# Kernel tuning notes

Hardware: AMD Instinct MI355X
Metric: run time of the kernel (lower is better)

The kernel has to match this reference:

```python
import jax, jax.numpy as jnp
import numpy as np

R_ITER = 3
EPS = 1e-7  # keras.backend.epsilon()


def squash(v, axis=-1):
    s2 = jnp.sum(jnp.square(v), axis=axis, keepdims=True)
    scale = s2 / (1.0 + s2) / jnp.sqrt(s2 + EPS)
    return scale * v


def setup_inputs() -> dict:
    key = jax.random.key(0)
    kx, kw = jax.random.split(key)
    B, N_IN, D_IN = 64, 2048, 8
    N_OUT, D_OUT = 32, 16
    x = jax.random.normal(kx, (B, N_IN, D_IN), dtype=jnp.float32)
    # W matches keras weight (1, N_IN//shared, N_OUT, D_OUT, D_IN) with shared=1,
    # stored here without the leading broadcast dim. RandomNormal(stddev=0.1).
    W = 0.1 * jax.random.normal(kw, (N_IN, N_OUT, D_OUT, D_IN), dtype=jnp.float32)
    return {"x": x, "W": W}


def reference(x, W):
    # predictions u_hat[b, i, j, :] = W[i, j] @ x[b, i]  -> [B, N_in, N_out, D_out]
    preds = jnp.einsum('nodi,bni->bnod', W, x)
    N_in, N_out = preds.shape[1], preds.shape[2]
    # raw routing logits start at zeros with broadcast batch dim (as in TF code)
    raw = jnp.zeros((1, N_in, N_out), dtype=x.dtype)
    for i in range(R_ITER):
        rw = jax.nn.softmax(raw, axis=2)                      # softmax over output caps
        s = jnp.sum(rw[..., None] * preds, axis=1)            # [B, N_out, D_out]
        v = squash(s, axis=-1)                                # squash over capsule dim
        if i < R_ITER - 1:
            # agreement: <u_hat_ij, v_j>
            raw = raw + jnp.einsum('bnod,bod->bno', preds, v)
    return v, rw
```

## Files before the change

kernel.cpp:

```cpp
#include <hip/hip_runtime.h>

static constexpr int B_    = 64;
static constexpr int N_    = 2048;
static constexpr int DI_   = 8;
static constexpr int O_    = 32;
static constexpr int P_    = 16;
static constexpr int OP_   = O_ * P_;
static constexpr int M_    = OP_ * B_;
static constexpr int CHUNK_ = 8;
static constexpr int NBLK_  = N_ / CHUNK_;
static constexpr int WSLICE_ = O_ * P_ * DI_;

template <int CTRL>
__device__ __forceinline__ float dpp_add(float v) {
  int t = __builtin_amdgcn_update_dpp(0, __float_as_int(v), CTRL, 0xf, 0xf, false);
  return v + __int_as_float(t);
}

__device__ __forceinline__ float rfl(float v) {
  return __int_as_float(__builtin_amdgcn_readfirstlane(__float_as_int(v)));
}

template <int MODE, bool ATOMIC>
__global__ __launch_bounds__(512, 2)
void fused_pass(const float* __restrict__ x, const float* __restrict__ W,
                const float* __restrict__ v_in, float* __restrict__ s_out,
                float* __restrict__ rw_out) {
  __shared__ __align__(16) float w_lds[WSLICE_];
  const int tid  = threadIdx.x;
  const int lane = tid & 63;
  const int wu   = __builtin_amdgcn_readfirstlane(tid >> 6);
  const int o    = lane >> 1;
  const int ph   = lane & 1;
  const int cn   = blockIdx.x >> 1;
  const int bh   = blockIdx.x & 1;
  const int n0   = cn * CHUNK_;
  const int b0   = bh * 32 + wu * 4;

  const int t2  = tid + 512;
  const int sw0 = (tid ^ ((tid >> 4) & 7)) * 4;
  const int sw1 = (t2  ^ ((t2  >> 4) & 7)) * 4;
  const int wbase = lane * 64 + (lane & 7) * 4;

  float s_r[4][8];
  #pragma unroll
  for (int bb = 0; bb < 4; ++bb)
    #pragma unroll
    for (int pp = 0; pp < 8; ++pp) s_r[bb][pp] = 0.0f;

  {
    const float4 a = *(const float4*)(W + (size_t)n0 * WSLICE_ + tid * 4);
    const float4 b = *(const float4*)(W + (size_t)n0 * WSLICE_ + t2 * 4);
    *(float4*)&w_lds[sw0] = a;
    *(float4*)&w_lds[sw1] = b;
  }
  __syncthreads();

  #pragma unroll 1
  for (int nn = 0; nn < CHUNK_; ++nn) {
    const int n = n0 + nn;

    float4 wrA, wrB;
    if (nn + 1 < CHUNK_) {
      wrA = *(const float4*)(W + (size_t)(n + 1) * WSLICE_ + tid * 4);
      wrB = *(const float4*)(W + (size_t)(n + 1) * WSLICE_ + t2 * 4);
    }

    float xs[4][8];
    #pragma unroll
    for (int bb = 0; bb < 4; ++bb) {
      const float* xp = x + (size_t)(b0 + bb) * (N_ * DI_) + (size_t)n * DI_;
      const float4 xa = *(const float4*)xp;
      const float4 xc = *(const float4*)(xp + 4);
      xs[bb][0] = rfl(xa.x); xs[bb][1] = rfl(xa.y);
      xs[bb][2] = rfl(xa.z); xs[bb][3] = rfl(xa.w);
      xs[bb][4] = rfl(xc.x); xs[bb][5] = rfl(xc.y);
      xs[bb][6] = rfl(xc.z); xs[bb][7] = rfl(xc.w);
    }

    float pr[4][8];
    #pragma unroll
    for (int pp = 0; pp < 8; ++pp) {
      const float4 w0 = *(const float4*)&w_lds[wbase ^ (8 * pp)];
      const float4 w1 = *(const float4*)&w_lds[wbase ^ (8 * pp + 4)];
      #pragma unroll
      for (int bb = 0; bb < 4; ++bb) {
        float pv = w0.x * xs[bb][0];
        pv = __builtin_fmaf(w0.y, xs[bb][1], pv);
        pv = __builtin_fmaf(w0.z, xs[bb][2], pv);
        pv = __builtin_fmaf(w0.w, xs[bb][3], pv);
        pv = __builtin_fmaf(w1.x, xs[bb][4], pv);
        pv = __builtin_fmaf(w1.y, xs[bb][5], pv);
        pv = __builtin_fmaf(w1.z, xs[bb][6], pv);
        pv = __builtin_fmaf(w1.w, xs[bb][7], pv);
        if (MODE == 0) s_r[bb][pp] += pv;
        else           pr[bb][pp] = pv;
      }
    }

    if (MODE != 0) {
      #pragma unroll
      for (int bb = 0; bb < 4; ++bb) {
        const float4* vp = (const float4*)(v_in + (size_t)(b0 + bb) * OP_ +
                                           o * P_ + ph * 8);
        const float4 va = vp[0];
        const float4 vc = vp[1];
        float acc = pr[bb][0] * va.x;
        acc = __builtin_fmaf(pr[bb][1], va.y, acc);
        acc = __builtin_fmaf(pr[bb][2], va.z, acc);
        acc = __builtin_fmaf(pr[bb][3], va.w, acc);
        acc = __builtin_fmaf(pr[bb][4], vc.x, acc);
        acc = __builtin_fmaf(pr[bb][5], vc.y, acc);
        acc = __builtin_fmaf(pr[bb][6], vc.z, acc);
        acc = __builtin_fmaf(pr[bb][7], vc.w, acc);
        const float full = dpp_add<0xB1>(acc);
        const float e = __expf(full);
        float srow = e;
        srow = dpp_add<0x121>(srow);
        srow = dpp_add<0x122>(srow);
        srow = dpp_add<0x124>(srow);
        srow = dpp_add<0x128>(srow);
        float t16 = srow + __shfl_xor(srow, 16);
        const float S = t16 + __shfl_xor(t16, 32);
        const float rw = (2.0f * e) / S;
        #pragma unroll
        for (int pp = 0; pp < 8; ++pp)
          s_r[bb][pp] = __builtin_fmaf(rw, pr[bb][pp], s_r[bb][pp]);
        if (MODE == 2) {
          if (ph == 0)
            rw_out[((size_t)(b0 + bb) * N_ + n) * O_ + o] = rw;
        }
      }
    }

    if (nn + 1 < CHUNK_) {
      __syncthreads();
      *(float4*)&w_lds[sw0] = wrA;
      *(float4*)&w_lds[sw1] = wrB;
      __syncthreads();
    }
  }

  if (ATOMIC) {
    #pragma unroll
    for (int bb = 0; bb < 4; ++bb) {
      #pragma unroll
      for (int h = 0; h < 2; ++h)
        #pragma unroll
        for (int j = 0; j < 4; ++j)
          atomicAdd(&s_out[(size_t)(b0 + bb) * 512 + h * 256 + lane * 4 + j],
                    s_r[bb][h * 4 + j]);
    }
  } else {
    #pragma unroll
    for (int bb = 0; bb < 4; ++bb) {
      float* sp = s_out + (size_t)cn * M_ + (size_t)(b0 + bb) * 512 + lane * 4;
      float4 st0, st1;
      st0.x = s_r[bb][0]; st0.y = s_r[bb][1]; st0.z = s_r[bb][2]; st0.w = s_r[bb][3];
      st1.x = s_r[bb][4]; st1.y = s_r[bb][5]; st1.z = s_r[bb][6]; st1.w = s_r[bb][7];
      *(float4*)sp = st0;
      *(float4*)(sp + 256) = st1;
    }
  }
}

__global__ __launch_bounds__(1024)
void reduce1(const float* __restrict__ spart, float* __restrict__ p2, int K) {
  const int g  = blockIdx.x >> 4;
  const int mc = blockIdx.x & 15;
  const int kpg = K >> 4;
  const int m0 = mc * 2048 + threadIdx.x;
  float a0 = 0.0f, a1 = 0.0f;
  const float* p = spart + (size_t)(g * kpg) * M_;
  for (int k = 0; k < kpg; ++k) {
    a0 += p[(size_t)k * M_ + m0];
    a1 += p[(size_t)k * M_ + m0 + 1024];
  }
  p2[(size_t)g * M_ + m0]        = a0;
  p2[(size_t)g * M_ + m0 + 1024] = a1;
}

__global__ __launch_bounds__(1024)
void v_kernel(const float* __restrict__ src, int ngroups, float scale,
              const float* __restrict__ v_add, float* __restrict__ v_out,
              float* __restrict__ zero_buf) {
  __shared__ float sq[P_ * 65];
  const int t = threadIdx.x;
  const int p = t & 15;
  const int b = t >> 4;
  const int o = blockIdx.x;
  const int q = o * P_ + p;
  const int idx_src = b * 512 + ((p >> 2) & 1) * 256 + (2 * o + (p >> 3)) * 4 +
                      (p & 3);
  float acc = 0.0f;
  for (int g = 0; g < ngroups; ++g)
    acc += src[(size_t)g * M_ + idx_src];
  acc *= scale;
  sq[p * 65 + b] = acc * acc;
  if (zero_buf) zero_buf[blockIdx.x * 1024 + t] = 0.0f;
  __syncthreads();
  float s2 = 0.0f;
  #pragma unroll
  for (int pp = 0; pp < P_; ++pp) s2 += sq[pp * 65 + b];
  float sc = (s2 / (1.0f + s2)) / sqrtf(s2 + 1e-7f);
  float v = acc * sc;
  const int idx = b * OP_ + q;
  v_out[idx] = v + (v_add ? v_add[idx] : 0.0f);
}

extern "C" void kernel_launch(void* const* d_in, const int* in_sizes, int n_in,
                              void* d_out, int out_size, void* d_ws, size_t ws_size,
                              hipStream_t stream) {
  (void)in_sizes; (void)n_in; (void)out_size;
  const float* x = (const float*)d_in[0];
  const float* W = (const float*)d_in[1];
  float* out_v  = (float*)d_out;
  float* out_rw = out_v + (size_t)B_ * O_ * P_;
  float* vws   = (float*)d_ws;
  float* vsum  = vws + M_;
  float* p2    = vsum + M_;
  float* spart = p2 + 16 * M_;

  const size_t need = (size_t)(2 * M_ + 16 * M_ + (size_t)NBLK_ * M_) * 4;

  dim3 gF(2 * NBLK_), bF(512), gV(O_), bV(1024), gR(256), bR(1024);
  if (ws_size >= need) {
    fused_pass<0, false><<<gF, bF, 0, stream>>>(x, W, nullptr, spart, nullptr);
    reduce1<<<gR, bR, 0, stream>>>(spart, p2, NBLK_);
    v_kernel<<<gV, bV, 0, stream>>>(p2, 16, 1.0f / 32.0f, nullptr, vws, nullptr);
    fused_pass<1, false><<<gF, bF, 0, stream>>>(x, W, vws, spart, nullptr);
    reduce1<<<gR, bR, 0, stream>>>(spart, p2, NBLK_);
    v_kernel<<<gV, bV, 0, stream>>>(p2, 16, 1.0f, vws, vsum, nullptr);
    fused_pass<2, false><<<gF, bF, 0, stream>>>(x, W, vsum, spart, out_rw);
    reduce1<<<gR, bR, 0, stream>>>(spart, p2, NBLK_);
    v_kernel<<<gV, bV, 0, stream>>>(p2, 16, 1.0f, nullptr, out_v, nullptr);
  } else {
    float* sAb = p2;
    float* sBb = sAb + M_;
    hipMemsetAsync(sAb, 0, (size_t)M_ * sizeof(float), stream);
    fused_pass<0, true><<<gF, bF, 0, stream>>>(x, W, nullptr, sAb, nullptr);
    v_kernel<<<gV, bV, 0, stream>>>(sAb, 1, 1.0f / 32.0f, nullptr, vws, sBb);
    fused_pass<1, true><<<gF, bF, 0, stream>>>(x, W, vws, sBb, nullptr);
    v_kernel<<<gV, bV, 0, stream>>>(sBb, 1, 1.0f, vws, vsum, sAb);
    fused_pass<2, true><<<gF, bF, 0, stream>>>(x, W, vsum, sAb, out_rw);
    v_kernel<<<gV, bV, 0, stream>>>(sAb, 1, 1.0f, nullptr, out_v, nullptr);
  }
}
```

Measured before the change: 224.6 us.

## Double-buffer W in LDS, stage x in LDS, split batch into quarters

Each block now has 256 threads and covers a quarter of the batch, so the grid has four times as many blocks. The W slice is double-buffered in LDS, which drops one of the two barriers per iteration. Each block's x tile is loaded into LDS once up front instead of being read from global memory every iteration, and the v_in loads are hoisted ahead of the dot products. In exchange, each W slice is fetched by four blocks instead of two, and LDS use per block roughly doubles, which could limit occupancy.

```diff
diff --git a/kernel.cpp b/kernel.cpp
--- a/kernel.cpp
+++ b/kernel.cpp
@@ -22,24 +22,24 @@
 }
 
 template <int MODE, bool ATOMIC>
-__global__ __launch_bounds__(512, 2)
+__global__ __launch_bounds__(256, 4)
 void fused_pass(const float* __restrict__ x, const float* __restrict__ W,
                 const float* __restrict__ v_in, float* __restrict__ s_out,
                 float* __restrict__ rw_out) {
-  __shared__ __align__(16) float w_lds[WSLICE_];
+  __shared__ __align__(16) float w_lds[2][WSLICE_];
+  __shared__ __align__(16) float x_lds[16 * 64];
   const int tid  = threadIdx.x;
   const int lane = tid & 63;
   const int wu   = __builtin_amdgcn_readfirstlane(tid >> 6);
   const int o    = lane >> 1;
   const int ph   = lane & 1;
-  const int cn   = blockIdx.x >> 1;
-  const int bh   = blockIdx.x & 1;
+  const int cn   = blockIdx.x >> 2;
+  const int bq   = blockIdx.x & 3;
   const int n0   = cn * CHUNK_;
-  const int b0   = bh * 32 + wu * 4;
-
-  const int t2  = tid + 512;
-  const int sw0 = (tid ^ ((tid >> 4) & 7)) * 4;
-  const int sw1 = (t2  ^ ((t2  >> 4) & 7)) * 4;
+  const int b0_blk = bq * 16;
+  const int b0w  = b0_blk + wu * 4;
+
+  const int swk = (tid ^ ((tid >> 4) & 7)) * 4;
   const int wbase = lane * 64 + (lane & 7) * 4;
 
   float s_r[4][8];
@@ -49,29 +49,41 @@
     for (int pp = 0; pp < 8; ++pp) s_r[bb][pp] = 0.0f;
 
   {
-    const float4 a = *(const float4*)(W + (size_t)n0 * WSLICE_ + tid * 4);
-    const float4 b = *(const float4*)(W + (size_t)n0 * WSLICE_ + t2 * 4);
-    *(float4*)&w_lds[sw0] = a;
-    *(float4*)&w_lds[sw1] = b;
+    const int bl = tid >> 4;
+    const int ch = tid & 15;
+    const float4 xv = *(const float4*)(
+        x + (size_t)(b0_blk + bl) * (N_ * DI_) + n0 * DI_ + ch * 4);
+    *(float4*)&x_lds[bl * 64 + ch * 4] = xv;
+    #pragma unroll
+    for (int k = 0; k < 4; ++k) {
+      const float4 wv =
+          *(const float4*)(W + (size_t)n0 * WSLICE_ + (tid + k * 256) * 4);
+      *(float4*)&w_lds[0][swk + k * 1024] = wv;
+    }
   }
   __syncthreads();
 
   #pragma unroll 1
   for (int nn = 0; nn < CHUNK_; ++nn) {
     const int n = n0 + nn;
-
-    float4 wrA, wrB;
+    const float* wbuf = w_lds[nn & 1];
+    float* wnxt = w_lds[(nn + 1) & 1];
+
+    float4 wr0, wr1, wr2, wr3;
     if (nn + 1 < CHUNK_) {
-      wrA = *(const float4*)(W + (size_t)(n + 1) * WSLICE_ + tid * 4);
-      wrB = *(const float4*)(W + (size_t)(n + 1) * WSLICE_ + t2 * 4);
+      const float* wp = W + (size_t)(n + 1) * WSLICE_ + tid * 4;
+      wr0 = *(const float4*)(wp);
+      wr1 = *(const float4*)(wp + 1024);
+      wr2 = *(const float4*)(wp + 2048);
+      wr3 = *(const float4*)(wp + 3072);
     }
 
     float xs[4][8];
     #pragma unroll
     for (int bb = 0; bb < 4; ++bb) {
-      const float* xp = x + (size_t)(b0 + bb) * (N_ * DI_) + (size_t)n * DI_;
-      const float4 xa = *(const float4*)xp;
-      const float4 xc = *(const float4*)(xp + 4);
+      const int xb = (wu * 4 + bb) * 64 + nn * 8;
+      const float4 xa = *(const float4*)&x_lds[xb];
+      const float4 xc = *(const float4*)&x_lds[xb + 4];
       xs[bb][0] = rfl(xa.x); xs[bb][1] = rfl(xa.y);
       xs[bb][2] = rfl(xa.z); xs[bb][3] = rfl(xa.w);
       xs[bb][4] = rfl(xc.x); xs[bb][5] = rfl(xc.y);
@@ -81,8 +93,8 @@
     float pr[4][8];
     #pragma unroll
     for (int pp = 0; pp < 8; ++pp) {
-      const float4 w0 = *(const float4*)&w_lds[wbase ^ (8 * pp)];
-      const float4 w1 = *(const float4*)&w_lds[wbase ^ (8 * pp + 4)];
+      const float4 w0 = *(const float4*)&wbuf[wbase ^ (8 * pp)];
+      const float4 w1 = *(const float4*)&wbuf[wbase ^ (8 * pp + 4)];
       #pragma unroll
       for (int bb = 0; bb < 4; ++bb) {
         float pv = w0.x * xs[bb][0];
@@ -99,20 +111,24 @@
     }
 
     if (MODE != 0) {
+      float4 va[4], vc[4];
       #pragma unroll
       for (int bb = 0; bb < 4; ++bb) {
-        const float4* vp = (const float4*)(v_in + (size_t)(b0 + bb) * OP_ +
-                                           o * P_ + ph * 8);
-        const float4 va = vp[0];
-        const float4 vc = vp[1];
-        float acc = pr[bb][0] * va.x;
-        acc = __builtin_fmaf(pr[bb][1], va.y, acc);
-        acc = __builtin_fmaf(pr[bb][2], va.z, acc);
-        acc = __builtin_fmaf(pr[bb][3], va.w, acc);
-        acc = __builtin_fmaf(pr[bb][4], vc.x, acc);
-        acc = __builtin_fmaf(pr[bb][5], vc.y, acc);
-        acc = __builtin_fmaf(pr[bb][6], vc.z, acc);
-        acc = __builtin_fmaf(pr[bb][7], vc.w, acc);
+        const float4* vp =
+            (const float4*)(v_in + (size_t)(b0w + bb) * OP_ + lane * 8);
+        va[bb] = vp[0];
+        vc[bb] = vp[1];
+      }
+      #pragma unroll
+      for (int bb = 0; bb < 4; ++bb) {
+        float acc = pr[bb][0] * va[bb].x;
+        acc = __builtin_fmaf(pr[bb][1], va[bb].y, acc);
+        acc = __builtin_fmaf(pr[bb][2], va[bb].z, acc);
+        acc = __builtin_fmaf(pr[bb][3], va[bb].w, acc);
+        acc = __builtin_fmaf(pr[bb][4], vc[bb].x, acc);
+        acc = __builtin_fmaf(pr[bb][5], vc[bb].y, acc);
+        acc = __builtin_fmaf(pr[bb][6], vc[bb].z, acc);
+        acc = __builtin_fmaf(pr[bb][7], vc[bb].w, acc);
         const float full = dpp_add<0xB1>(acc);
         const float e = __expf(full);
         float srow = e;
@@ -128,15 +144,16 @@
           s_r[bb][pp] = __builtin_fmaf(rw, pr[bb][pp], s_r[bb][pp]);
         if (MODE == 2) {
           if (ph == 0)
-            rw_out[((size_t)(b0 + bb) * N_ + n) * O_ + o] = rw;
+            rw_out[((size_t)(b0w + bb) * N_ + n) * O_ + o] = rw;
         }
       }
     }
 
     if (nn + 1 < CHUNK_) {
-      __syncthreads();
-      *(float4*)&w_lds[sw0] = wrA;
-      *(float4*)&w_lds[sw1] = wrB;
+      *(float4*)&wnxt[swk]        = wr0;
+      *(float4*)&wnxt[swk + 1024] = wr1;
+      *(float4*)&wnxt[swk + 2048] = wr2;
+      *(float4*)&wnxt[swk + 3072] = wr3;
       __syncthreads();
     }
   }
@@ -148,13 +165,13 @@
       for (int h = 0; h < 2; ++h)
         #pragma unroll
         for (int j = 0; j < 4; ++j)
-          atomicAdd(&s_out[(size_t)(b0 + bb) * 512 + h * 256 + lane * 4 + j],
+          atomicAdd(&s_out[(size_t)(b0w + bb) * 512 + h * 256 + lane * 4 + j],
                     s_r[bb][h * 4 + j]);
     }
   } else {
     #pragma unroll
     for (int bb = 0; bb < 4; ++bb) {
-      float* sp = s_out + (size_t)cn * M_ + (size_t)(b0 + bb) * 512 + lane * 4;
+      float* sp = s_out + (size_t)cn * M_ + (size_t)(b0w + bb) * 512 + lane * 4;
       float4 st0, st1;
       st0.x = s_r[bb][0]; st0.y = s_r[bb][1]; st0.z = s_r[bb][2]; st0.w = s_r[bb][3];
       st1.x = s_r[bb][4]; st1.y = s_r[bb][5]; st1.z = s_r[bb][6]; st1.w = s_r[bb][7];
@@ -223,7 +240,7 @@
 
   const size_t need = (size_t)(2 * M_ + 16 * M_ + (size_t)NBLK_ * M_) * 4;
 
-  dim3 gF(2 * NBLK_), bF(512), gV(O_), bV(1024), gR(256), bR(1024);
+  dim3 gF(4 * NBLK_), bF(256), gV(O_), bV(1024), gR(256), bR(1024);
   if (ws_size >= need) {
     fused_pass<0, false><<<gF, bF, 0, stream>>>(x, W, nullptr, spart, nullptr);
     reduce1<<<gR, bR, 0, stream>>>(spart, p2, NBLK_);
```

After: 323.0 us. 43.8% more time.

## Replace partial-sum buffers and reduce kernel with 16-way atomic groups, 4-stage W ring

Applied to the files above, without the earlier changes.

Removes the per-block partial-sum writes and the separate reduce1 kernel. Each fused pass now atomically accumulates into one of 16 group buffers, which the v_kernel sums and re-zeroes for the next pass. The W slice staging becomes a 4-deep LDS ring with prefetch two iterations ahead, so there is one barrier per two n-steps instead of two per step. The v vector is hoisted into registers once per block. This cuts launches and global traffic but adds atomic contention and LDS usage that may lower occupancy.

```diff
diff --git a/kernel.cpp b/kernel.cpp
--- a/kernel.cpp
+++ b/kernel.cpp
@@ -21,12 +21,12 @@
   return __int_as_float(__builtin_amdgcn_readfirstlane(__float_as_int(v)));
 }
 
-template <int MODE, bool ATOMIC>
+template <int MODE>
 __global__ __launch_bounds__(512, 2)
 void fused_pass(const float* __restrict__ x, const float* __restrict__ W,
-                const float* __restrict__ v_in, float* __restrict__ s_out,
-                float* __restrict__ rw_out) {
-  __shared__ __align__(16) float w_lds[WSLICE_];
+                const float* __restrict__ v_in, float* __restrict__ p2,
+                float* __restrict__ rw_out, int gmask) {
+  __shared__ __align__(16) float w_lds[4][WSLICE_];
   const int tid  = threadIdx.x;
   const int lane = tid & 63;
   const int wu   = __builtin_amdgcn_readfirstlane(tid >> 6);
@@ -35,12 +35,22 @@
   const int cn   = blockIdx.x >> 1;
   const int bh   = blockIdx.x & 1;
   const int n0   = cn * CHUNK_;
-  const int b0   = bh * 32 + wu * 4;
-
-  const int t2  = tid + 512;
-  const int sw0 = (tid ^ ((tid >> 4) & 7)) * 4;
-  const int sw1 = (t2  ^ ((t2  >> 4) & 7)) * 4;
+  const int b0w  = bh * 32 + wu * 4;
+
+  const int swk   = (tid ^ ((tid >> 4) & 7)) * 4;
   const int wbase = lane * 64 + (lane & 7) * 4;
+
+  float vv[4][8];
+  if (MODE != 0) {
+    #pragma unroll
+    for (int bb = 0; bb < 4; ++bb) {
+      const float4* vp =
+          (const float4*)(v_in + (size_t)(b0w + bb) * OP_ + lane * 8);
+      const float4 a = vp[0], c = vp[1];
+      vv[bb][0] = a.x; vv[bb][1] = a.y; vv[bb][2] = a.z; vv[bb][3] = a.w;
+      vv[bb][4] = c.x; vv[bb][5] = c.y; vv[bb][6] = c.z; vv[bb][7] = c.w;
+    }
+  }
 
   float s_r[4][8];
   #pragma unroll
@@ -49,141 +59,124 @@
     for (int pp = 0; pp < 8; ++pp) s_r[bb][pp] = 0.0f;
 
   {
-    const float4 a = *(const float4*)(W + (size_t)n0 * WSLICE_ + tid * 4);
-    const float4 b = *(const float4*)(W + (size_t)n0 * WSLICE_ + t2 * 4);
-    *(float4*)&w_lds[sw0] = a;
-    *(float4*)&w_lds[sw1] = b;
+    const float* wp = W + (size_t)n0 * WSLICE_;
+    const float4 a0 = *(const float4*)(wp + tid * 4);
+    const float4 a1 = *(const float4*)(wp + tid * 4 + 2048);
+    const float4 b0 = *(const float4*)(wp + WSLICE_ + tid * 4);
+    const float4 b1 = *(const float4*)(wp + WSLICE_ + tid * 4 + 2048);
+    *(float4*)&w_lds[0][swk]        = a0;
+    *(float4*)&w_lds[0][swk + 2048] = a1;
+    *(float4*)&w_lds[1][swk]        = b0;
+    *(float4*)&w_lds[1][swk + 2048] = b1;
   }
   __syncthreads();
 
   #pragma unroll 1
-  for (int nn = 0; nn < CHUNK_; ++nn) {
-    const int n = n0 + nn;
-
-    float4 wrA, wrB;
-    if (nn + 1 < CHUNK_) {
-      wrA = *(const float4*)(W + (size_t)(n + 1) * WSLICE_ + tid * 4);
-      wrB = *(const float4*)(W + (size_t)(n + 1) * WSLICE_ + t2 * 4);
-    }
-
-    float xs[4][8];
-    #pragma unroll
-    for (int bb = 0; bb < 4; ++bb) {
-      const float* xp = x + (size_t)(b0 + bb) * (N_ * DI_) + (size_t)n * DI_;
-      const float4 xa = *(const float4*)xp;
-      const float4 xc = *(const float4*)(xp + 4);
-      xs[bb][0] = rfl(xa.x); xs[bb][1] = rfl(xa.y);
-      xs[bb][2] = rfl(xa.z); xs[bb][3] = rfl(xa.w);
-      xs[bb][4] = rfl(xc.x); xs[bb][5] = rfl(xc.y);
-      xs[bb][6] = rfl(xc.z); xs[bb][7] = rfl(xc.w);
-    }
-
-    float pr[4][8];
-    #pragma unroll
-    for (int pp = 0; pp < 8; ++pp) {
-      const float4 w0 = *(const float4*)&w_lds[wbase ^ (8 * pp)];
-      const float4 w1 = *(const float4*)&w_lds[wbase ^ (8 * pp + 4)];
+  for (int nn = 0; nn < CHUNK_; nn += 2) {
+    #pragma unroll
+    for (int u = 0; u < 2; ++u) {
+      const int n = n0 + nn + u;
+      const float* wbuf = &w_lds[(nn + u) & 3][0];
+      const int pf = nn + 2 + u;
+
+      float4 c0, c1;
+      if (pf < CHUNK_) {
+        const float* wp = W + (size_t)(n0 + pf) * WSLICE_;
+        c0 = *(const float4*)(wp + tid * 4);
+        c1 = *(const float4*)(wp + tid * 4 + 2048);
+      }
+
+      float xs[4][8];
       #pragma unroll
       for (int bb = 0; bb < 4; ++bb) {
-        float pv = w0.x * xs[bb][0];
-        pv = __builtin_fmaf(w0.y, xs[bb][1], pv);
-        pv = __builtin_fmaf(w0.z, xs[bb][2], pv);
-        pv = __builtin_fmaf(w0.w, xs[bb][3], pv);
-        pv = __builtin_fmaf(w1.x, xs[bb][4], pv);
-        pv = __builtin_fmaf(w1.y, xs[bb][5], pv);
-        pv = __builtin_fmaf(w1.z, xs[bb][6], pv);
-        pv = __builtin_fmaf(w1.w, xs[bb][7], pv);
-        if (MODE == 0) s_r[bb][pp] += pv;
-        else           pr[bb][pp] = pv;
+        const float* xp =
+            x + (size_t)(b0w + bb) * (N_ * DI_) + (size_t)n * DI_;
+        const float4 xa = *(const float4*)xp;
+        const float4 xc = *(const float4*)(xp + 4);
+        xs[bb][0] = rfl(xa.x); xs[bb][1] = rfl(xa.y);
+        xs[bb][2] = rfl(xa.z); xs[bb][3] = rfl(xa.w);
+        xs[bb][4] = rfl(xc.x); xs[bb][5] = rfl(xc.y);
+        xs[bb][6] = rfl(xc.z); xs[bb][7] = rfl(xc.w);
+      }
+
+      float pr[4][8];
+      #pragma unroll
+      for (int pp = 0; pp < 8; ++pp) {
+        const float4 w0 = *(const float4*)&wbuf[wbase ^ (8 * pp)];
+        const float4 w1 = *(const float4*)&wbuf[wbase ^ (8 * pp + 4)];
+        #pragma unroll
+        for (int bb = 0; bb < 4; ++bb) {
+          float pv = w0.x * xs[bb][0];
+          pv = __builtin_fmaf(w0.y, xs[bb][1], pv);
+          pv = __builtin_fmaf(w0.z, xs[bb][2], pv);
+          pv = __builtin_fmaf(w0.w, xs[bb][3], pv);
+          pv = __builtin_fmaf(w1.x, xs[bb][4], pv);
+          pv = __builtin_fmaf(w1.y, xs[bb][5], pv);
+          pv = __builtin_fmaf(w1.z, xs[bb][6], pv);
+          pv = __builtin_fmaf(w1.w, xs[bb][7], pv);
+          if (MODE == 0) s_r[bb][pp] += pv;
+          else           pr[bb][pp] = pv;
+        }
+      }
+
+      if (MODE != 0) {
+        #pragma unroll
+        for (int bb = 0; bb < 4; ++bb) {
+          float acc = pr[bb][0] * vv[bb][0];
+          acc = __builtin_fmaf(pr[bb][1], vv[bb][1], acc);
+          acc = __builtin_fmaf(pr[bb][2], vv[bb][2], acc);
+          acc = __builtin_fmaf(pr[bb][3], vv[bb][3], acc);
+          acc = __builtin_fmaf(pr[bb][4], vv[bb][4], acc);
+          acc = __builtin_fmaf(pr[bb][5], vv[bb][5], acc);
+          acc = __builtin_fmaf(pr[bb][6], vv[bb][6], acc);
+          acc = __builtin_fmaf(pr[bb][7], vv[bb][7], acc);
+          const float full = dpp_add<0xB1>(acc);
+          const float e = __expf(full);
+          float srow = e;
+          srow = dpp_add<0x121>(srow);
+          srow = dpp_add<0x122>(srow);
+          srow = dpp_add<0x124>(srow);
+          srow = dpp_add<0x128>(srow);
+          float t16 = srow + __shfl_xor(srow, 16);
+          const float S = t16 + __shfl_xor(t16, 32);
+          const float rw = (2.0f * e) / S;
+          #pragma unroll
+          for (int pp = 0; pp < 8; ++pp)
+            s_r[bb][pp] = __builtin_fmaf(rw, pr[bb][pp], s_r[bb][pp]);
+          if (MODE == 2) {
+            if (ph == 0)
+              rw_out[((size_t)(b0w + bb) * N_ + n) * O_ + o] = rw;
+          }
+        }
+      }
+
+      if (pf < CHUNK_) {
+        float* dst = &w_lds[pf & 3][0];
+        *(float4*)&dst[swk]        = c0;
+        *(float4*)&dst[swk + 2048] = c1;
       }
     }
-
-    if (MODE != 0) {
-      #pragma unroll
-      for (int bb = 0; bb < 4; ++bb) {
-        const float4* vp = (const float4*)(v_in + (size_t)(b0 + bb) * OP_ +
-                                           o * P_ + ph * 8);
-        const float4 va = vp[0];
-        const float4 vc = vp[1];
-        float acc = pr[bb][0] * va.x;
-        acc = __builtin_fmaf(pr[bb][1], va.y, acc);
-        acc = __builtin_fmaf(pr[bb][2], va.z, acc);
-        acc = __builtin_fmaf(pr[bb][3], va.w, acc);
-        acc = __builtin_fmaf(pr[bb][4], vc.x, acc);
-        acc = __builtin_fmaf(pr[bb][5], vc.y, acc);
-        acc = __builtin_fmaf(pr[bb][6], vc.z, acc);
-        acc = __builtin_fmaf(pr[bb][7], vc.w, acc);
-        const float full = dpp_add<0xB1>(acc);
-        const float e = __expf(full);
-        float srow = e;
-        srow = dpp_add<0x121>(srow);
-        srow = dpp_add<0x122>(srow);
-        srow = dpp_add<0x124>(srow);
-        srow = dpp_add<0x128>(srow);
-        float t16 = srow + __shfl_xor(srow, 16);
-        const float S = t16 + __shfl_xor(t16, 32);
-        const float rw = (2.0f * e) / S;
-        #pragma unroll
-        for (int pp = 0; pp < 8; ++pp)
-          s_r[bb][pp] = __builtin_fmaf(rw, pr[bb][pp], s_r[bb][pp]);
-        if (MODE == 2) {
-          if (ph == 0)
-            rw_out[((size_t)(b0 + bb) * N_ + n) * O_ + o] = rw;
-        }
-      }
-    }
-
-    if (nn + 1 < CHUNK_) {
-      __syncthreads();
-      *(float4*)&w_lds[sw0] = wrA;
-      *(float4*)&w_lds[sw1] = wrB;
-      __syncthreads();
-    }
-  }
-
-  if (ATOMIC) {
+    __syncthreads();
+  }
+
+  {
+    float* basep = p2 + (size_t)(cn & gmask) * M_;
     #pragma unroll
     for (int bb = 0; bb < 4; ++bb) {
+      float* sp = basep + (size_t)(b0w + bb) * 512 + lane * 4;
       #pragma unroll
       for (int h = 0; h < 2; ++h)
         #pragma unroll
         for (int j = 0; j < 4; ++j)
-          atomicAdd(&s_out[(size_t)(b0 + bb) * 512 + h * 256 + lane * 4 + j],
-                    s_r[bb][h * 4 + j]);
+          atomicAdd(&sp[h * 256 + j], s_r[bb][h * 4 + j]);
     }
-  } else {
-    #pragma unroll
-    for (int bb = 0; bb < 4; ++bb) {
-      float* sp = s_out + (size_t)cn * M_ + (size_t)(b0 + bb) * 512 + lane * 4;
-      float4 st0, st1;
-      st0.x = s_r[bb][0]; st0.y = s_r[bb][1]; st0.z = s_r[bb][2]; st0.w = s_r[bb][3];
-      st1.x = s_r[bb][4]; st1.y = s_r[bb][5]; st1.z = s_r[bb][6]; st1.w = s_r[bb][7];
-      *(float4*)sp = st0;
-      *(float4*)(sp + 256) = st1;
-    }
-  }
-}
-
-__global__ __launch_bounds__(1024)
-void reduce1(const float* __restrict__ spart, float* __restrict__ p2, int K) {
-  const int g  = blockIdx.x >> 4;
-  const int mc = blockIdx.x & 15;
-  const int kpg = K >> 4;
-  const int m0 = mc * 2048 + threadIdx.x;
-  float a0 = 0.0f, a1 = 0.0f;
-  const float* p = spart + (size_t)(g * kpg) * M_;
-  for (int k = 0; k < kpg; ++k) {
-    a0 += p[(size_t)k * M_ + m0];
-    a1 += p[(size_t)k * M_ + m0 + 1024];
-  }
-  p2[(size_t)g * M_ + m0]        = a0;
-  p2[(size_t)g * M_ + m0 + 1024] = a1;
+  }
 }
 
 __global__ __launch_bounds__(1024)
 void v_kernel(const float* __restrict__ src, int ngroups, float scale,
               const float* __restrict__ v_add, float* __restrict__ v_out,
-              float* __restrict__ zero_buf) {
+              float* __restrict__ zero_buf, int zgroups) {
   __shared__ float sq[P_ * 65];
   const int t = threadIdx.x;
   const int p = t & 15;
@@ -197,7 +190,10 @@
     acc += src[(size_t)g * M_ + idx_src];
   acc *= scale;
   sq[p * 65 + b] = acc * acc;
-  if (zero_buf) zero_buf[blockIdx.x * 1024 + t] = 0.0f;
+  if (zero_buf) {
+    for (int g = 0; g < zgroups; ++g)
+      zero_buf[(size_t)g * M_ + blockIdx.x * 1024 + t] = 0.0f;
+  }
   __syncthreads();
   float s2 = 0.0f;
   #pragma unroll
@@ -218,31 +214,29 @@
   float* out_rw = out_v + (size_t)B_ * O_ * P_;
   float* vws   = (float*)d_ws;
   float* vsum  = vws + M_;
-  float* p2    = vsum + M_;
-  float* spart = p2 + 16 * M_;
-
-  const size_t need = (size_t)(2 * M_ + 16 * M_ + (size_t)NBLK_ * M_) * 4;
-
-  dim3 gF(2 * NBLK_), bF(512), gV(O_), bV(1024), gR(256), bR(1024);
-  if (ws_size >= need) {
-    fused_pass<0, false><<<gF, bF, 0, stream>>>(x, W, nullptr, spart, nullptr);
-    reduce1<<<gR, bR, 0, stream>>>(spart, p2, NBLK_);
-    v_kernel<<<gV, bV, 0, stream>>>(p2, 16, 1.0f / 32.0f, nullptr, vws, nullptr);
-    fused_pass<1, false><<<gF, bF, 0, stream>>>(x, W, vws, spart, nullptr);
-    reduce1<<<gR, bR, 0, stream>>>(spart, p2, NBLK_);
-    v_kernel<<<gV, bV, 0, stream>>>(p2, 16, 1.0f, vws, vsum, nullptr);
-    fused_pass<2, false><<<gF, bF, 0, stream>>>(x, W, vsum, spart, out_rw);
-    reduce1<<<gR, bR, 0, stream>>>(spart, p2, NBLK_);
-    v_kernel<<<gV, bV, 0, stream>>>(p2, 16, 1.0f, nullptr, out_v, nullptr);
+
+  dim3 gF(2 * NBLK_), bF(512), gV(O_), bV(1024);
+
+  const size_t need_big = (size_t)(2 * M_ + 32 * M_) * sizeof(float);
+  if (ws_size >= need_big) {
+    float* p2A = vsum + M_;
+    float* p2B = p2A + 16 * M_;
+    hipMemsetAsync(p2A, 0, (size_t)16 * M_ * sizeof(float), stream);
+    fused_pass<0><<<gF, bF, 0, stream>>>(x, W, nullptr, p2A, nullptr, 15);
+    v_kernel<<<gV, bV, 0, stream>>>(p2A, 16, 1.0f / 32.0f, nullptr, vws, p2B, 16);
+    fused_pass<1><<<gF, bF, 0, stream>>>(x, W, vws, p2B, nullptr, 15);
+    v_kernel<<<gV, bV, 0, stream>>>(p2B, 16, 1.0f, vws, vsum, p2A, 16);
+    fused_pass<2><<<gF, bF, 0, stream>>>(x, W, vsum, p2A, out_rw, 15);
+    v_kernel<<<gV, bV, 0, stream>>>(p2A, 16, 1.0f, nullptr, out_v, nullptr, 0);
   } else {
-    float* sAb = p2;
-    float* sBb = sAb + M_;
-    hipMemsetAsync(sAb, 0, (size_t)M_ * sizeof(float), stream);
-    fused_pass<0, true><<<gF, bF, 0, stream>>>(x, W, nullptr, sAb, nullptr);
-    v_kernel<<<gV, bV, 0, stream>>>(sAb, 1, 1.0f / 32.0f, nullptr, vws, sBb);
-    fused_pass<1, true><<<gF, bF, 0, stream>>>(x, W, vws, sBb, nullptr);
-    v_kernel<<<gV, bV, 0, stream>>>(sBb, 1, 1.0f, vws, vsum, sAb);
-    fused_pass<2, true><<<gF, bF, 0, stream>>>(x, W, vsum, sAb, out_rw);
-    v_kernel<<<gV, bV, 0, stream>>>(sAb, 1, 1.0f, nullptr, out_v, nullptr);
-  }
-}
+    float* sA = vsum + M_;
+    float* sB = sA + M_;
+    hipMemsetAsync(sA, 0, (size_t)M_ * sizeof(float), stream);
+    fused_pass<0><<<gF, bF, 0, stream>>>(x, W, nullptr, sA, nullptr, 0);
+    v_kernel<<<gV, bV, 0, stream>>>(sA, 1, 1.0f / 32.0f, nullptr, vws, sB, 1);
+    fused_pass<1><<<gF, bF, 0, stream>>>(x, W, vws, sB, nullptr, 0);
+    v_kernel<<<gV, bV, 0, stream>>>(sB, 1, 1.0f, vws, vsum, sA, 1);
+    fused_pass<2><<<gF, bF, 0, stream>>>(x, W, vsum, sA, out_rw, 0);
+    v_kernel<<<gV, bV, 0, stream>>>(sA, 1, 1.0f, nullptr, out_v, nullptr, 0);
+  }
+}
```

New measurement: 474.5 us. 111% more time.
